# Kernel optimization log

Measured on AMD Instinct MI355X. Metric: run time of the kernel, lower is better.

## Reference

```python
import jax, jax.numpy as jnp
import numpy as np

N_NODES = 100000
N_EDGES = 1600000
N_GRAPHS = 2000
IN_DIM = 37
HID = 128
OUT_CLS = 2


def _leconv(x, src, dst, w, W1, b1, W2, W3, b3):
    # PyG LEConv: out[i] = sum_j w_ij * (lin1(x)[i] - lin2(x)[j]) + lin3(x)[i]
    a = x @ W1 + b1          # [N, H]
    b = x @ W2               # [N, H] (lin2 has no bias)
    c = x @ W3 + b3          # [N, H]
    deg = jax.ops.segment_sum(w, dst, num_segments=N_NODES)              # [N]
    agg = jax.ops.segment_sum(w[:, None] * b[src], dst, num_segments=N_NODES)  # [N, H]
    return deg[:, None] * a - agg + c


def setup_inputs() -> dict:
    key = jax.random.key(0)
    ks = jax.random.split(key, 32)
    inp = {}
    inp["x"] = jax.random.normal(ks[0], (N_NODES, IN_DIM), dtype=jnp.float32)
    inp["edge_index"] = jax.random.randint(ks[1], (2, N_EDGES), 0, N_NODES, dtype=jnp.int64)
    inp["batch"] = jnp.sort(jax.random.randint(ks[2], (N_NODES,), 0, N_GRAPHS, dtype=jnp.int64))
    dims = [(IN_DIM, HID), (HID, HID), (HID, HID)]
    ki = 3
    for l, (di, do) in enumerate(dims):
        s = 1.0 / np.sqrt(di)
        inp[f"W1_{l}"] = jax.random.uniform(ks[ki + 0], (di, do), jnp.float32, -s, s)
        inp[f"b1_{l}"] = jax.random.uniform(ks[ki + 1], (do,), jnp.float32, -s, s)
        inp[f"W2_{l}"] = jax.random.uniform(ks[ki + 2], (di, do), jnp.float32, -s, s)
        inp[f"W3_{l}"] = jax.random.uniform(ks[ki + 3], (di, do), jnp.float32, -s, s)
        inp[f"b3_{l}"] = jax.random.uniform(ks[ki + 4], (do,), jnp.float32, -s, s)
        ki += 5
    sf = 1.0 / np.sqrt(HID)
    inp["Wf1"] = jax.random.uniform(ks[ki + 0], (HID, HID), jnp.float32, -sf, sf)
    inp["bf1"] = jax.random.uniform(ks[ki + 1], (HID,), jnp.float32, -sf, sf)
    inp["Wf2"] = jax.random.uniform(ks[ki + 2], (HID, OUT_CLS), jnp.float32, -sf, sf)
    inp["bf2"] = jax.random.uniform(ks[ki + 3], (OUT_CLS,), jnp.float32, -sf, sf)
    return inp


def reference(x, edge_index, batch,
              W1_0, b1_0, W2_0, W3_0, b3_0,
              W1_1, b1_1, W2_1, W3_1, b3_1,
              W1_2, b1_2, W2_2, W3_2, b3_2,
              Wf1, bf1, Wf2, bf2):
    src, dst = edge_index[0], edge_index[1]
    w = jnp.ones((edge_index.shape[1],), dtype=x.dtype)  # edge_weight = ones
    layers = [(W1_0, b1_0, W2_0, W3_0, b3_0),
              (W1_1, b1_1, W2_1, W3_1, b3_1),
              (W1_2, b1_2, W2_2, W3_2, b3_2)]
    h = x
    for (W1, b1, W2, W3, b3) in layers:
        h = jax.nn.relu(_leconv(h, src, dst, w, W1, b1, W2, W3, b3))
    # global mean pool per graph
    sums = jax.ops.segment_sum(h, batch, num_segments=N_GRAPHS)           # [G, H]
    cnt = jax.ops.segment_sum(jnp.ones((N_NODES,), h.dtype), batch, num_segments=N_GRAPHS)
    graph_x = sums / jnp.clip(cnt, 1.0)[:, None]
    # FFN head (Dropout is identity at inference)
    pred = jax.nn.relu(graph_x @ Wf1 + bf1) @ Wf2 + bf2                   # [G, 2]
    return pred
```

## Files before the change

### kernel.cpp

```cpp
#include <hip/hip_runtime.h>
#include <hip/hip_bf16.h>
#include <cstdint>

#define N_NODES 100000
#define N_EDGES 1600000
#define N_GRAPHS 2000
#define IN_DIM 37
#define HID 128

#define GEMM_GRID 1563
#define HIST_BLOCKS 6250
#define PACK_BLOCKS 480
#define CSTRIDE 80

typedef __attribute__((ext_vector_type(8))) short short8;
typedef __attribute__((ext_vector_type(4))) float f32x4;

static __device__ __forceinline__ short bf16_bits(float f) {
    __hip_bfloat16 h = __float2bfloat16(f);
    return *reinterpret_cast<short*>(&h);
}
static __device__ __forceinline__ float bf16_lo(uint32_t u) {
    uint32_t v = u << 16;
    return *reinterpret_cast<float*>(&v);
}
static __device__ __forceinline__ float bf16_hi(uint32_t u) {
    uint32_t v = u & 0xffff0000u;
    return *reinterpret_cast<float*>(&v);
}
static __device__ __forceinline__ uint32_t pack_bf16(float lo, float hi) {
    return ((uint32_t)(uint16_t)bf16_bits(hi) << 16) | (uint16_t)bf16_bits(lo);
}


struct PackArgs {
    const float* w[9];
    short* o[9];
};

static __device__ __forceinline__ void pack_one(const PackArgs& pa, int m, int r, int kin) {
    const int i = r & 7, lane = (r >> 3) & 63, t = (r >> 9) & 7, kb = r >> 12;
    const int k = kb * 32 + (lane >> 4) * 8 + i;
    const int c = t * 16 + (lane & 15);
    float v = (k < kin) ? pa.w[m][(size_t)k * HID + c] : 0.f;
    pa.o[m][r] = bf16_bits(v);
}


__global__ __launch_bounds__(256) void phase1_kernel(const int* __restrict__ ei,
                                                     int* __restrict__ cnt,
                                                     int* __restrict__ colp,
                                                     PackArgs pa) {
    const int b = blockIdx.x;
    if (b < HIST_BLOCKS) {
        const int e = b * 256 + threadIdx.x;
        const int s = ei[e];
        const int d = ei[N_EDGES + e];
        const int rk = atomicAdd(&cnt[d], 1);
        if (rk < CSTRIDE) colp[(size_t)d * CSTRIDE + rk] = s;
        return;
    }
    const int idx = (b - HIST_BLOCKS) * 256 + threadIdx.x;
    if (idx < 24576) pack_one(pa, idx >> 13, idx & 8191, IN_DIM);
    else { const int q = idx - 24576; pack_one(pa, 3 + (q >> 14), q & 16383, HID); }
}


__global__ __launch_bounds__(256) void gemm0_kernel(
    const float* __restrict__ x,
    const short* __restrict__ Wp1, const short* __restrict__ Wp2, const short* __restrict__ Wp3,
    const float* __restrict__ b1v, const float* __restrict__ b3v,
    short* __restrict__ D0, short* __restrict__ E0, short* __restrict__ Bb) {
    const int tid = threadIdx.x;
    const int wave = tid >> 6, lane = tid & 63;
    const int row_base = blockIdx.x * 64 + wave * 16;
    const int r15 = lane & 15, kg = lane >> 4;
    int arow = row_base + r15;
    if (arow >= N_NODES) arow = N_NODES - 1;
    const float* xr = x + (size_t)arow * IN_DIM;

    f32x4 acc1[8], acc2[8], acc3[8];
    #pragma unroll
    for (int t = 0; t < 8; t++) {
        acc1[t] = (f32x4)0.f; acc2[t] = (f32x4)0.f; acc3[t] = (f32x4)0.f;
    }
    #pragma unroll
    for (int kb = 0; kb < 2; kb++) {
        short8 av;
        #pragma unroll
        for (int i = 0; i < 8; i++) {
            const int k = kb * 32 + kg * 8 + i;
            av[i] = (k < IN_DIM) ? bf16_bits(xr[k]) : (short)0;
        }
        #pragma unroll
        for (int t = 0; t < 8; t++) {
            const int widx = (kb * 8 + t) * 512 + lane * 8;
            short8 w1 = *(const short8*)(Wp1 + widx);
            short8 w2 = *(const short8*)(Wp2 + widx);
            short8 w3 = *(const short8*)(Wp3 + widx);
            acc1[t] = __builtin_amdgcn_mfma_f32_16x16x32_bf16(av, w1, acc1[t], 0, 0, 0);
            acc2[t] = __builtin_amdgcn_mfma_f32_16x16x32_bf16(av, w2, acc2[t], 0, 0, 0);
            acc3[t] = __builtin_amdgcn_mfma_f32_16x16x32_bf16(av, w3, acc3[t], 0, 0, 0);
        }
    }
    int grow[4]; bool ok[4];
    #pragma unroll
    for (int i = 0; i < 4; i++) {
        grow[i] = row_base + kg * 4 + i;
        ok[i] = grow[i] < N_NODES;
    }
    #pragma unroll
    for (int t = 0; t < 8; t++) {
        const int c = t * 16 + r15;
        const float bb1 = b1v[c], bb3 = b3v[c];
        #pragma unroll
        for (int i = 0; i < 4; i++) {
            if (ok[i]) {
                size_t o = (size_t)grow[i] * HID + c;
                D0[o] = bf16_bits(acc1[t][i] + bb1);
                E0[o] = bf16_bits(acc3[t][i] + bb3);
                Bb[o] = bf16_bits(acc2[t][i]);
            }
        }
    }
}


static __device__ __forceinline__ void agg_edges4(const int* __restrict__ colbase, int e,
                                                  const short* __restrict__ Bb,
                                                  int lane, int grp, int l16, float* acc) {
    for (int base = 0; base < e; base += 64) {
        const int cnt = min(64, e - base);
        const int ci = base + lane;
        const int cv = colbase[(ci < e) ? ci : (e - 1)];
        for (int t = 0; t < cnt; t += 4) {
            const int idx = t + grp;
            const bool on = idx < cnt;
            const float w = on ? 1.f : 0.f;
            const int c = __shfl(cv, on ? idx : 0, 64);
            const uint4 u = *(const uint4*)(Bb + (size_t)c * HID + l16 * 8);
            acc[0] = fmaf(w, bf16_lo(u.x), acc[0]);
            acc[1] = fmaf(w, bf16_hi(u.x), acc[1]);
            acc[2] = fmaf(w, bf16_lo(u.y), acc[2]);
            acc[3] = fmaf(w, bf16_hi(u.y), acc[3]);
            acc[4] = fmaf(w, bf16_lo(u.z), acc[4]);
            acc[5] = fmaf(w, bf16_hi(u.z), acc[5]);
            acc[6] = fmaf(w, bf16_lo(u.w), acc[6]);
            acc[7] = fmaf(w, bf16_hi(u.w), acc[7]);
        }
    }
    #pragma unroll
    for (int j = 0; j < 8; j++) {
        acc[j] += __shfl_xor(acc[j], 16, 64);
        acc[j] += __shfl_xor(acc[j], 32, 64);
    }
}

__global__ __launch_bounds__(256) void gather0_kernel(const int* __restrict__ cnt,
                                                      const int* __restrict__ colp,
                                                      const short* __restrict__ Bb,
                                                      const short* __restrict__ D0,
                                                      const short* __restrict__ E0,
                                                      short* __restrict__ Hb) {
    const int wid = (blockIdx.x * 256 + threadIdx.x) >> 6;
    if (wid >= N_NODES) return;
    const int lane = threadIdx.x & 63, grp = lane >> 4, l16 = lane & 15;
    const int deg = cnt[wid];
    const int e = min(deg, CSTRIDE);
    float acc[8] = {0.f, 0.f, 0.f, 0.f, 0.f, 0.f, 0.f, 0.f};
    agg_edges4(colp + (size_t)wid * CSTRIDE, e, Bb, lane, grp, l16, acc);
    if (grp == 0) {
        const float dg = (float)deg;
        const uint4 ud = *(const uint4*)(D0 + (size_t)wid * HID + l16 * 8);
        const uint4 ue = *(const uint4*)(E0 + (size_t)wid * HID + l16 * 8);
        uint4 r;
        r.x = pack_bf16(fmaxf(fmaf(dg, bf16_lo(ud.x), bf16_lo(ue.x)) - acc[0], 0.f),
                        fmaxf(fmaf(dg, bf16_hi(ud.x), bf16_hi(ue.x)) - acc[1], 0.f));
        r.y = pack_bf16(fmaxf(fmaf(dg, bf16_lo(ud.y), bf16_lo(ue.y)) - acc[2], 0.f),
                        fmaxf(fmaf(dg, bf16_hi(ud.y), bf16_hi(ue.y)) - acc[3], 0.f));
        r.z = pack_bf16(fmaxf(fmaf(dg, bf16_lo(ud.z), bf16_lo(ue.z)) - acc[4], 0.f),
                        fmaxf(fmaf(dg, bf16_hi(ud.z), bf16_hi(ue.z)) - acc[5], 0.f));
        r.w = pack_bf16(fmaxf(fmaf(dg, bf16_lo(ud.w), bf16_lo(ue.w)) - acc[6], 0.f),
                        fmaxf(fmaf(dg, bf16_hi(ud.w), bf16_hi(ue.w)) - acc[7], 0.f));
        *(uint4*)(Hb + (size_t)wid * HID + l16 * 8) = r;
    }
}

__global__ __launch_bounds__(256) void gatherL_kernel(const int* __restrict__ cnt,
                                                      const int* __restrict__ colp,
                                                      const short* __restrict__ Bb,
                                                      const short* __restrict__ OUTb,
                                                      short* __restrict__ Hb) {
    const int wid = (blockIdx.x * 256 + threadIdx.x) >> 6;
    if (wid >= N_NODES) return;
    const int lane = threadIdx.x & 63, grp = lane >> 4, l16 = lane & 15;
    const int e = min(cnt[wid], CSTRIDE);
    float acc[8] = {0.f, 0.f, 0.f, 0.f, 0.f, 0.f, 0.f, 0.f};
    agg_edges4(colp + (size_t)wid * CSTRIDE, e, Bb, lane, grp, l16, acc);
    if (grp == 0) {
        const uint4 uo = *(const uint4*)(OUTb + (size_t)wid * HID + l16 * 8);
        uint4 r;
        r.x = pack_bf16(fmaxf(bf16_lo(uo.x) - acc[0], 0.f), fmaxf(bf16_hi(uo.x) - acc[1], 0.f));
        r.y = pack_bf16(fmaxf(bf16_lo(uo.y) - acc[2], 0.f), fmaxf(bf16_hi(uo.y) - acc[3], 0.f));
        r.z = pack_bf16(fmaxf(bf16_lo(uo.z) - acc[4], 0.f), fmaxf(bf16_hi(uo.z) - acc[5], 0.f));
        r.w = pack_bf16(fmaxf(bf16_lo(uo.w) - acc[6], 0.f), fmaxf(bf16_hi(uo.w) - acc[7], 0.f));
        *(uint4*)(Hb + (size_t)wid * HID + l16 * 8) = r;
    }
}


__global__ __launch_bounds__(256) void leconv_mfma(
    const short* __restrict__ Hb,
    const short* __restrict__ Wp1, const short* __restrict__ Wp2, const short* __restrict__ Wp3,
    const float* __restrict__ b1v, const float* __restrict__ b3v,
    const int* __restrict__ cnt,
    short* __restrict__ Bb, short* __restrict__ OUTb) {
    const int tid = threadIdx.x;
    const int wave = tid >> 6, lane = tid & 63;
    const int row_base = blockIdx.x * 64 + wave * 16;
    const int r15 = lane & 15, kg = lane >> 4;
    int arow = row_base + r15;
    if (arow >= N_NODES) arow = N_NODES - 1;
    const short* aptr = Hb + (size_t)arow * HID + kg * 8;

    f32x4 acc1[8], acc2[8], acc3[8];
    #pragma unroll
    for (int t = 0; t < 8; t++) {
        acc1[t] = (f32x4)0.f; acc2[t] = (f32x4)0.f; acc3[t] = (f32x4)0.f;
    }
    #pragma unroll
    for (int kb = 0; kb < 4; kb++) {
        short8 av = *(const short8*)(aptr + kb * 32);
        #pragma unroll
        for (int t = 0; t < 8; t++) {
            const int widx = (kb * 8 + t) * 512 + lane * 8;
            short8 w1 = *(const short8*)(Wp1 + widx);
            short8 w2 = *(const short8*)(Wp2 + widx);
            short8 w3 = *(const short8*)(Wp3 + widx);
            acc1[t] = __builtin_amdgcn_mfma_f32_16x16x32_bf16(av, w1, acc1[t], 0, 0, 0);
            acc2[t] = __builtin_amdgcn_mfma_f32_16x16x32_bf16(av, w2, acc2[t], 0, 0, 0);
            acc3[t] = __builtin_amdgcn_mfma_f32_16x16x32_bf16(av, w3, acc3[t], 0, 0, 0);
        }
    }
    int grow[4]; bool ok[4]; float dg[4];
    #pragma unroll
    for (int i = 0; i < 4; i++) {
        grow[i] = row_base + kg * 4 + i;
        ok[i] = grow[i] < N_NODES;
        dg[i] = ok[i] ? (float)cnt[grow[i]] : 0.f;
    }
    #pragma unroll
    for (int t = 0; t < 8; t++) {
        const int c = t * 16 + r15;
        const float bb1 = b1v[c], bb3 = b3v[c];
        #pragma unroll
        for (int i = 0; i < 4; i++) {
            if (ok[i]) {
                size_t o = (size_t)grow[i] * HID + c;
                OUTb[o] = bf16_bits(dg[i] * (acc1[t][i] + bb1) + acc3[t][i] + bb3);
                Bb[o] = bf16_bits(acc2[t][i]);
            }
        }
    }
}


__global__ __launch_bounds__(128) void pool_ffn_kernel(const short* __restrict__ H,
                                                       const int* __restrict__ batch,
                                                       const float* __restrict__ Wf1,
                                                       const float* __restrict__ bf1,
                                                       const float* __restrict__ Wf2,
                                                       const float* __restrict__ bf2,
                                                       float* __restrict__ out) {
    const int g = blockIdx.x;
    const int t = threadIdx.x;

    int lo = 0, hi = N_NODES;
    while (lo < hi) { int mid = (lo + hi) >> 1; if (batch[mid] < g) lo = mid + 1; else hi = mid; }
    const int s = lo;
    hi = N_NODES;
    while (lo < hi) { int mid = (lo + hi) >> 1; if (batch[mid] < g + 1) lo = mid + 1; else hi = mid; }
    const int e = lo;

    float sum = 0.f;
    for (int n = s; n < e; n++) {
        short b = H[(size_t)n * HID + t];
        sum += __bfloat162float(*(__hip_bfloat16*)&b);
    }
    const float cntf = (float)(e - s);
    const float gx = sum / fmaxf(cntf, 1.f);

    __shared__ float lds[HID];
    lds[t] = gx;
    __syncthreads();

    float hsum = bf1[t];
    #pragma unroll 8
    for (int k = 0; k < HID; k++) hsum = fmaf(lds[k], Wf1[k * HID + t], hsum);
    const float hr = fmaxf(hsum, 0.f);

    float p0 = hr * Wf2[t * 2 + 0];
    float p1 = hr * Wf2[t * 2 + 1];
    #pragma unroll
    for (int off = 32; off > 0; off >>= 1) {
        p0 += __shfl_down(p0, off, 64);
        p1 += __shfl_down(p1, off, 64);
    }
    __shared__ float red[4];
    if ((t & 63) == 0) {
        red[(t >> 6) * 2 + 0] = p0;
        red[(t >> 6) * 2 + 1] = p1;
    }
    __syncthreads();
    if (t == 0) {
        out[g * 2 + 0] = red[0] + red[2] + bf2[0];
        out[g * 2 + 1] = red[1] + red[3] + bf2[1];
    }
}


extern "C" void kernel_launch(void* const* d_in, const int* in_sizes, int n_in,
                              void* d_out, int out_size, void* d_ws, size_t ws_size,
                              hipStream_t stream) {
    (void)in_sizes; (void)n_in; (void)out_size; (void)ws_size;

    const float* x     = (const float*)d_in[0];
    const int*   ei    = (const int*)d_in[1];
    const int*   batch = (const int*)d_in[2];
    const float* W[9] = {
        (const float*)d_in[3],  (const float*)d_in[5],  (const float*)d_in[6],
        (const float*)d_in[8],  (const float*)d_in[10], (const float*)d_in[11],
        (const float*)d_in[13], (const float*)d_in[15], (const float*)d_in[16]};
    const float* b1_0 = (const float*)d_in[4];
    const float* b3_0 = (const float*)d_in[7];
    const float* b1_1 = (const float*)d_in[9];
    const float* b3_1 = (const float*)d_in[12];
    const float* b1_2 = (const float*)d_in[14];
    const float* b3_2 = (const float*)d_in[17];
    const float* Wf1  = (const float*)d_in[18];
    const float* bf1  = (const float*)d_in[19];
    const float* Wf2  = (const float*)d_in[20];
    const float* bf2  = (const float*)d_in[21];
    float* out = (float*)d_out;

    char* ws = (char*)d_ws;
    size_t off = 0;
    auto alloc = [&](size_t bytes) {
        void* p = ws + off;
        off += (bytes + 255) & ~(size_t)255;
        return p;
    };
    short* D0     = (short*)alloc((size_t)N_NODES * HID * 2);
    short* E0     = (short*)alloc((size_t)N_NODES * HID * 2);
    short* Bb_A   = (short*)alloc((size_t)N_NODES * HID * 2);
    short* Bb_B   = (short*)alloc((size_t)N_NODES * HID * 2);
    short* Hb     = (short*)alloc((size_t)N_NODES * HID * 2);
    int*   cnt    = (int*)alloc((size_t)N_NODES * 4);
    int*   colp   = (int*)alloc((size_t)N_NODES * CSTRIDE * 4);
    short* P[9];
    for (int m = 0; m < 9; m++) P[m] = (short*)alloc(16384 * 2);

    hipMemsetAsync(cnt, 0, (size_t)N_NODES * 4, stream);

    PackArgs pa;
    for (int m = 0; m < 9; m++) { pa.w[m] = W[m]; pa.o[m] = P[m]; }

    phase1_kernel<<<HIST_BLOCKS + PACK_BLOCKS, 256, 0, stream>>>(ei, cnt, colp, pa);

    gemm0_kernel<<<GEMM_GRID, 256, 0, stream>>>(x, P[0], P[1], P[2], b1_0, b3_0, D0, E0, Bb_A);

    const int gather_grid = (N_NODES * 64 + 255) / 256;

    gather0_kernel<<<gather_grid, 256, 0, stream>>>(cnt, colp, Bb_A, D0, E0, Hb);
    leconv_mfma<<<GEMM_GRID, 256, 0, stream>>>(Hb, P[3], P[4], P[5], b1_1, b3_1, cnt, Bb_B, E0);
    gatherL_kernel<<<gather_grid, 256, 0, stream>>>(cnt, colp, Bb_B, E0, Hb);
    leconv_mfma<<<GEMM_GRID, 256, 0, stream>>>(Hb, P[6], P[7], P[8], b1_2, b3_2, cnt, Bb_A, D0);
    gatherL_kernel<<<gather_grid, 256, 0, stream>>>(cnt, colp, Bb_A, D0, Hb);

    pool_ffn_kernel<<<N_GRAPHS, 128, 0, stream>>>(Hb, batch, Wf1, bf1, Wf2, bf2, out);
}
```

Before: 517.3 us.

## Stage GEMM outputs through LDS for coalesced stores and split edge fill

```diff
diff --git a/kernel.cpp b/kernel.cpp
--- a/kernel.cpp
+++ b/kernel.cpp
@@ -49,15 +49,13 @@
 
 __global__ __launch_bounds__(256) void phase1_kernel(const int* __restrict__ ei,
                                                      int* __restrict__ cnt,
-                                                     int* __restrict__ colp,
+                                                     int* __restrict__ rank,
                                                      PackArgs pa) {
     const int b = blockIdx.x;
     if (b < HIST_BLOCKS) {
         const int e = b * 256 + threadIdx.x;
-        const int s = ei[e];
         const int d = ei[N_EDGES + e];
-        const int rk = atomicAdd(&cnt[d], 1);
-        if (rk < CSTRIDE) colp[(size_t)d * CSTRIDE + rk] = s;
+        rank[e] = atomicAdd(&cnt[d], 1);
         return;
     }
     const int idx = (b - HIST_BLOCKS) * 256 + threadIdx.x;
@@ -66,14 +64,31 @@
 }
 
 
-__global__ __launch_bounds__(256) void gemm0_kernel(
-    const float* __restrict__ x,
+static __device__ __forceinline__ void repack_store(short (*tile)[136],
+                                                    int kg, int r15, int row_base,
+                                                    short* __restrict__ dst) {
+    const int gnode = row_base + r15;
+    if (gnode < N_NODES) {
+        const int cbase = kg * 32;
+        #pragma unroll
+        for (int j = 0; j < 4; j++) {
+            const uint4 v = *(const uint4*)&tile[r15][cbase + j * 8];
+            *(uint4*)(dst + (size_t)gnode * HID + cbase + j * 8) = v;
+        }
+    }
+}
+
+
+static __device__ __forceinline__ void gemm0_body(
+    int blk, const float* __restrict__ x,
     const short* __restrict__ Wp1, const short* __restrict__ Wp2, const short* __restrict__ Wp3,
     const float* __restrict__ b1v, const float* __restrict__ b3v,
-    short* __restrict__ D0, short* __restrict__ E0, short* __restrict__ Bb) {
+    short* __restrict__ D0, short* __restrict__ E0, short* __restrict__ Bb,
+    short (*tile)[136]) {
     const int tid = threadIdx.x;
-    const int wave = tid >> 6, lane = tid & 63;
-    const int row_base = blockIdx.x * 64 + wave * 16;
+    const int lane = tid & 63;
+    const int wave = tid >> 6;
+    const int row_base = blk * 64 + wave * 16;
     const int r15 = lane & 15, kg = lane >> 4;
     int arow = row_base + r15;
     if (arow >= N_NODES) arow = N_NODES - 1;
@@ -103,26 +118,50 @@
             acc3[t] = __builtin_amdgcn_mfma_f32_16x16x32_bf16(av, w3, acc3[t], 0, 0, 0);
         }
     }
-    int grow[4]; bool ok[4];
-    #pragma unroll
-    for (int i = 0; i < 4; i++) {
-        grow[i] = row_base + kg * 4 + i;
-        ok[i] = grow[i] < N_NODES;
-    }
     #pragma unroll
     for (int t = 0; t < 8; t++) {
         const int c = t * 16 + r15;
-        const float bb1 = b1v[c], bb3 = b3v[c];
-        #pragma unroll
-        for (int i = 0; i < 4; i++) {
-            if (ok[i]) {
-                size_t o = (size_t)grow[i] * HID + c;
-                D0[o] = bf16_bits(acc1[t][i] + bb1);
-                E0[o] = bf16_bits(acc3[t][i] + bb3);
-                Bb[o] = bf16_bits(acc2[t][i]);
-            }
-        }
-    }
+        const float bb1 = b1v[c];
+        #pragma unroll
+        for (int i = 0; i < 4; i++) tile[kg * 4 + i][c] = bf16_bits(acc1[t][i] + bb1);
+    }
+    repack_store(tile, kg, r15, row_base, D0);
+    #pragma unroll
+    for (int t = 0; t < 8; t++) {
+        const int c = t * 16 + r15;
+        const float bb3 = b3v[c];
+        #pragma unroll
+        for (int i = 0; i < 4; i++) tile[kg * 4 + i][c] = bf16_bits(acc3[t][i] + bb3);
+    }
+    repack_store(tile, kg, r15, row_base, E0);
+    #pragma unroll
+    for (int t = 0; t < 8; t++) {
+        const int c = t * 16 + r15;
+        #pragma unroll
+        for (int i = 0; i < 4; i++) tile[kg * 4 + i][c] = bf16_bits(acc2[t][i]);
+    }
+    repack_store(tile, kg, r15, row_base, Bb);
+}
+
+__global__ __launch_bounds__(256) void fill_gemm0_kernel(
+    const int* __restrict__ ei, const int* __restrict__ rank,
+    int* __restrict__ colp,
+    const float* __restrict__ x,
+    const short* __restrict__ Wp1, const short* __restrict__ Wp2, const short* __restrict__ Wp3,
+    const float* __restrict__ b1v, const float* __restrict__ b3v,
+    short* __restrict__ D0, short* __restrict__ E0, short* __restrict__ Bb) {
+    __shared__ short lds_t[4][16][136];
+    const int b = blockIdx.x;
+    if (b < HIST_BLOCKS) {
+        const int e = b * 256 + threadIdx.x;
+        const int s = ei[e];
+        const int d = ei[N_EDGES + e];
+        const int rk = rank[e];
+        if (rk < CSTRIDE) colp[(size_t)d * CSTRIDE + rk] = s;
+        return;
+    }
+    gemm0_body(b - HIST_BLOCKS, x, Wp1, Wp2, Wp3, b1v, b3v, D0, E0, Bb,
+               lds_t[threadIdx.x >> 6]);
 }
 
 
@@ -215,10 +254,12 @@
     const float* __restrict__ b1v, const float* __restrict__ b3v,
     const int* __restrict__ cnt,
     short* __restrict__ Bb, short* __restrict__ OUTb) {
+    __shared__ short lds_t[4][16][136];
     const int tid = threadIdx.x;
     const int wave = tid >> 6, lane = tid & 63;
     const int row_base = blockIdx.x * 64 + wave * 16;
     const int r15 = lane & 15, kg = lane >> 4;
+    short (*tile)[136] = lds_t[wave];
     int arow = row_base + r15;
     if (arow >= N_NODES) arow = N_NODES - 1;
     const short* aptr = Hb + (size_t)arow * HID + kg * 8;
@@ -242,26 +283,29 @@
             acc3[t] = __builtin_amdgcn_mfma_f32_16x16x32_bf16(av, w3, acc3[t], 0, 0, 0);
         }
     }
-    int grow[4]; bool ok[4]; float dg[4];
+    float dg[4];
     #pragma unroll
     for (int i = 0; i < 4; i++) {
-        grow[i] = row_base + kg * 4 + i;
-        ok[i] = grow[i] < N_NODES;
-        dg[i] = ok[i] ? (float)cnt[grow[i]] : 0.f;
+        const int gr = row_base + kg * 4 + i;
+        dg[i] = (gr < N_NODES) ? (float)cnt[gr] : 0.f;
     }
     #pragma unroll
     for (int t = 0; t < 8; t++) {
         const int c = t * 16 + r15;
         const float bb1 = b1v[c], bb3 = b3v[c];
         #pragma unroll
-        for (int i = 0; i < 4; i++) {
-            if (ok[i]) {
-                size_t o = (size_t)grow[i] * HID + c;
-                OUTb[o] = bf16_bits(dg[i] * (acc1[t][i] + bb1) + acc3[t][i] + bb3);
-                Bb[o] = bf16_bits(acc2[t][i]);
-            }
-        }
-    }
+        for (int i = 0; i < 4; i++)
+            tile[kg * 4 + i][c] = bf16_bits(dg[i] * (acc1[t][i] + bb1) + acc3[t][i] + bb3);
+    }
+    repack_store(tile, kg, r15, row_base, OUTb);
+    #pragma unroll
+    for (int t = 0; t < 8; t++) {
+        const int c = t * 16 + r15;
+        #pragma unroll
+        for (int i = 0; i < 4; i++)
+            tile[kg * 4 + i][c] = bf16_bits(acc2[t][i]);
+    }
+    repack_store(tile, kg, r15, row_base, Bb);
 }
 
 
@@ -356,6 +400,7 @@
     short* Bb_B   = (short*)alloc((size_t)N_NODES * HID * 2);
     short* Hb     = (short*)alloc((size_t)N_NODES * HID * 2);
     int*   cnt    = (int*)alloc((size_t)N_NODES * 4);
+    int*   rank   = (int*)alloc((size_t)N_EDGES * 4);
     int*   colp   = (int*)alloc((size_t)N_NODES * CSTRIDE * 4);
     short* P[9];
     for (int m = 0; m < 9; m++) P[m] = (short*)alloc(16384 * 2);
@@ -365,9 +410,10 @@
     PackArgs pa;
     for (int m = 0; m < 9; m++) { pa.w[m] = W[m]; pa.o[m] = P[m]; }
 
-    phase1_kernel<<<HIST_BLOCKS + PACK_BLOCKS, 256, 0, stream>>>(ei, cnt, colp, pa);
-
-    gemm0_kernel<<<GEMM_GRID, 256, 0, stream>>>(x, P[0], P[1], P[2], b1_0, b3_0, D0, E0, Bb_A);
+    phase1_kernel<<<HIST_BLOCKS + PACK_BLOCKS, 256, 0, stream>>>(ei, cnt, rank, pa);
+
+    fill_gemm0_kernel<<<HIST_BLOCKS + GEMM_GRID, 256, 0, stream>>>(
+        ei, rank, colp, x, P[0], P[1], P[2], b1_0, b3_0, D0, E0, Bb_A);
 
     const int gather_grid = (N_NODES * 64 + 255) / 256;
 
```

Result: faster. 473.1 us (-8.5%).

## Split edge histogram from column fill and unroll the gather loop

Applied to the files above, without the earlier changes.

```diff
diff --git a/kernel.cpp b/kernel.cpp
--- a/kernel.cpp
+++ b/kernel.cpp
@@ -49,15 +49,13 @@
 
 __global__ __launch_bounds__(256) void phase1_kernel(const int* __restrict__ ei,
                                                      int* __restrict__ cnt,
-                                                     int* __restrict__ colp,
+                                                     int* __restrict__ rank,
                                                      PackArgs pa) {
     const int b = blockIdx.x;
     if (b < HIST_BLOCKS) {
         const int e = b * 256 + threadIdx.x;
-        const int s = ei[e];
         const int d = ei[N_EDGES + e];
-        const int rk = atomicAdd(&cnt[d], 1);
-        if (rk < CSTRIDE) colp[(size_t)d * CSTRIDE + rk] = s;
+        rank[e] = atomicAdd(&cnt[d], 1);
         return;
     }
     const int idx = (b - HIST_BLOCKS) * 256 + threadIdx.x;
@@ -66,14 +64,14 @@
 }
 
 
-__global__ __launch_bounds__(256) void gemm0_kernel(
-    const float* __restrict__ x,
+static __device__ __forceinline__ void gemm0_body(
+    int blk, const float* __restrict__ x,
     const short* __restrict__ Wp1, const short* __restrict__ Wp2, const short* __restrict__ Wp3,
     const float* __restrict__ b1v, const float* __restrict__ b3v,
     short* __restrict__ D0, short* __restrict__ E0, short* __restrict__ Bb) {
     const int tid = threadIdx.x;
     const int wave = tid >> 6, lane = tid & 63;
-    const int row_base = blockIdx.x * 64 + wave * 16;
+    const int row_base = blk * 64 + wave * 16;
     const int r15 = lane & 15, kg = lane >> 4;
     int arow = row_base + r15;
     if (arow >= N_NODES) arow = N_NODES - 1;
@@ -126,6 +124,37 @@
 }
 
 
+__global__ __launch_bounds__(256) void fill_gemm0_kernel(
+    const int* __restrict__ ei, const int* __restrict__ rank,
+    int* __restrict__ colp,
+    const float* __restrict__ x,
+    const short* __restrict__ Wp1, const short* __restrict__ Wp2, const short* __restrict__ Wp3,
+    const float* __restrict__ b1v, const float* __restrict__ b3v,
+    short* __restrict__ D0, short* __restrict__ E0, short* __restrict__ Bb) {
+    const int b = blockIdx.x;
+    if (b < HIST_BLOCKS) {
+        const int e = b * 256 + threadIdx.x;
+        const int s = ei[e];
+        const int d = ei[N_EDGES + e];
+        const int rk = rank[e];
+        if (rk < CSTRIDE) colp[(size_t)d * CSTRIDE + rk] = s;
+        return;
+    }
+    gemm0_body(b - HIST_BLOCKS, x, Wp1, Wp2, Wp3, b1v, b3v, D0, E0, Bb);
+}
+
+
+static __device__ __forceinline__ void acc_row(const uint4& u, float* acc) {
+    acc[0] += bf16_lo(u.x);
+    acc[1] += bf16_hi(u.x);
+    acc[2] += bf16_lo(u.y);
+    acc[3] += bf16_hi(u.y);
+    acc[4] += bf16_lo(u.z);
+    acc[5] += bf16_hi(u.z);
+    acc[6] += bf16_lo(u.w);
+    acc[7] += bf16_hi(u.w);
+}
+
 static __device__ __forceinline__ void agg_edges4(const int* __restrict__ colbase, int e,
                                                   const short* __restrict__ Bb,
                                                   int lane, int grp, int l16, float* acc) {
@@ -133,7 +162,16 @@
         const int cnt = min(64, e - base);
         const int ci = base + lane;
         const int cv = colbase[(ci < e) ? ci : (e - 1)];
-        for (int t = 0; t < cnt; t += 4) {
+        int t = 0;
+        for (; t + 8 <= cnt; t += 8) {
+            const int c0 = __shfl(cv, t + grp, 64);
+            const int c1 = __shfl(cv, t + 4 + grp, 64);
+            const uint4 u0 = *(const uint4*)(Bb + (size_t)c0 * HID + l16 * 8);
+            const uint4 u1 = *(const uint4*)(Bb + (size_t)c1 * HID + l16 * 8);
+            acc_row(u0, acc);
+            acc_row(u1, acc);
+        }
+        for (; t < cnt; t += 4) {
             const int idx = t + grp;
             const bool on = idx < cnt;
             const float w = on ? 1.f : 0.f;
@@ -356,6 +394,7 @@
     short* Bb_B   = (short*)alloc((size_t)N_NODES * HID * 2);
     short* Hb     = (short*)alloc((size_t)N_NODES * HID * 2);
     int*   cnt    = (int*)alloc((size_t)N_NODES * 4);
+    int*   rank   = (int*)alloc((size_t)N_EDGES * 4);
     int*   colp   = (int*)alloc((size_t)N_NODES * CSTRIDE * 4);
     short* P[9];
     for (int m = 0; m < 9; m++) P[m] = (short*)alloc(16384 * 2);
@@ -365,9 +404,10 @@
     PackArgs pa;
     for (int m = 0; m < 9; m++) { pa.w[m] = W[m]; pa.o[m] = P[m]; }
 
-    phase1_kernel<<<HIST_BLOCKS + PACK_BLOCKS, 256, 0, stream>>>(ei, cnt, colp, pa);
-
-    gemm0_kernel<<<GEMM_GRID, 256, 0, stream>>>(x, P[0], P[1], P[2], b1_0, b3_0, D0, E0, Bb_A);
+    phase1_kernel<<<HIST_BLOCKS + PACK_BLOCKS, 256, 0, stream>>>(ei, cnt, rank, pa);
+
+    fill_gemm0_kernel<<<HIST_BLOCKS + GEMM_GRID, 256, 0, stream>>>(
+        ei, rank, colp, x, P[0], P[1], P[2], b1_0, b3_0, D0, E0, Bb_A);
 
     const int gather_grid = (N_NODES * 64 + 255) / 256;
 
```

Result: faster. 464.3 us (-10.3%).
